# Kernel tuning notes

Hardware: AMD Instinct MI355X
Metric: run time of the kernel (lower is better)

The kernel has to match this reference:

```python
import jax, jax.numpy as jnp
import numpy as np

STRIDES = [(2, 2), (3, 3), (4, 4)]
EPS = 1e-5


def _conv1x1(x, w, b):
    # x: [B,C,H,W], w: [O,C] -> [B,O,H,W]
    return jnp.einsum('bchw,oc->bohw', x, w) + b[None, :, None, None]


def _stitch(x, hs, ws):
    # x: [B,dk,H,W] -> patches [B, hs*ws, dk*oh*ow]; patch index = i*ws + j matches
    # torch.stack over itertools.product(range(hs), range(ws)) of x[:,:,i::hs,j::ws]
    b, dk, H, W = x.shape
    oh, ow = H // hs, W // ws
    p = x.reshape(b, dk, oh, hs, ow, ws).transpose(0, 3, 5, 1, 2, 4)  # [B,hs,ws,dk,oh,ow]
    return p.reshape(b, hs * ws, dk * oh * ow)


def _unstitch(y, b, dk, hs, ws, oh, ow):
    # faithful to the torch permute(0,3,1,4,2,5): H is assembled as (hs, oh), W as (ws, ow)
    y = y.reshape(b, hs, ws, dk, oh, ow).transpose(0, 3, 1, 4, 2, 5)  # [B,dk,hs,oh,ws,ow]
    return y.reshape(b, dk, hs * oh, ws * ow)


def _attention(q, k, v):
    d = q.shape[-1]
    scores = jnp.einsum('bpd,bqd->bpq', q, k) / jnp.sqrt(jnp.asarray(d, q.dtype))
    p = jax.nn.softmax(scores, axis=-1)
    return jnp.einsum('bpq,bqd->bpd', p, v)


def _forward(x, wq, bq, wk, bk, wv, bv, w_out, b_out, gamma, beta):
    b, c, h, w = x.shape
    n = len(STRIDES)
    dk = c // n
    q = _conv1x1(x, wq, bq)
    k = _conv1x1(x, wk, bk)
    v = _conv1x1(x, wv, bv)
    outs = []
    for idx, (ws_, hs_) in enumerate(STRIDES):
        sl = slice(idx * dk, (idx + 1) * dk)
        oh, ow = h // hs_, w // ws_
        qp = _stitch(q[:, sl], hs_, ws_)
        kp = _stitch(k[:, sl], hs_, ws_)
        vp = _stitch(v[:, sl], hs_, ws_)
        y = _attention(qp, kp, vp)  # [B, hs*ws, dk*oh*ow]
        outs.append(_unstitch(y, b, dk, hs_, ws_, oh, ow))
    out = jnp.concatenate(outs, axis=1)  # [B,C,H,W]
    # output_linear: Conv3x3 -> BatchNorm2d (training-mode batch stats) -> LeakyReLU(0.2)
    y = jax.lax.conv_general_dilated(out, w_out, (1, 1), 'SAME',
                                     dimension_numbers=('NCHW', 'OIHW', 'NCHW'))
    y = y + b_out[None, :, None, None]
    mean = jnp.mean(y, axis=(0, 2, 3), keepdims=True)
    var = jnp.var(y, axis=(0, 2, 3), keepdims=True)
    y = (y - mean) * jax.lax.rsqrt(var + EPS)
    y = y * gamma[None, :, None, None] + beta[None, :, None, None]
    return jnp.where(y >= 0, y, 0.2 * y)


def setup_inputs() -> dict:
    key = jax.random.key(0)
    ks = jax.random.split(key, 10)
    B, C, H, W = 16, 192, 96, 96
    s = 0.02
    return {
        'x': jax.random.normal(ks[0], (B, C, H, W), jnp.float32),
        'wq': jax.random.normal(ks[1], (C, C), jnp.float32) * s,
        'bq': jnp.zeros((C,), jnp.float32),
        'wk': jax.random.normal(ks[2], (C, C), jnp.float32) * s,
        'bk': jnp.zeros((C,), jnp.float32),
        'wv': jax.random.normal(ks[3], (C, C), jnp.float32) * s,
        'bv': jnp.zeros((C,), jnp.float32),
        'w_out': jax.random.normal(ks[4], (C, C, 3, 3), jnp.float32) * s,
        'b_out': jnp.zeros((C,), jnp.float32),
        'gamma': jnp.ones((C,), jnp.float32),
        'beta': jnp.zeros((C,), jnp.float32),
    }


def reference(x, wq, bq, wk, bk, wv, bv, w_out, b_out, gamma, beta):
    return _forward(x, wq, bq, wk, bk, wv, bv, w_out, b_out, gamma, beta)
```

## Files before the change

### kernel.cpp

```cpp
#include <hip/hip_runtime.h>
#include <hip/hip_bf16.h>

#define BB 16
#define CC 192
#define HH 96
#define WWW 96
#define HWSZ 9216
#define DKC 64

typedef __hip_bfloat16 bf16;
typedef __attribute__((ext_vector_type(8))) short s8v;
typedef __attribute__((ext_vector_type(4))) float f32x4;

__device__ __forceinline__ float bf2f(unsigned short u) {
  union { unsigned int i; float f; } x; x.i = ((unsigned int)u) << 16; return x.f;
}
__device__ __forceinline__ unsigned short f2bf(float f) {
  union { __hip_bfloat16 h; unsigned short u; } c; c.h = __float2bfloat16(f); return c.u;
}

__global__ __launch_bounds__(256) void prep_w_kernel(const float* __restrict__ w_out,
                                                     unsigned short* __restrict__ wb9T) {
  int e = blockIdx.x * 256 + threadIdx.x;
  if (e >= 9 * CC * CC) return;
  int c = e % CC;
  int oc = (e / CC) % CC;
  int sh = e / (CC * CC);
  wb9T[e] = f2bf(w_out[((size_t)(oc * CC + c)) * 9 + sh]);
}

__global__ __launch_bounds__(256) void prep_wqkv_kernel(
    const float* __restrict__ wq, const float* __restrict__ wk, const float* __restrict__ wv,
    unsigned short* __restrict__ wqkv) {
  int e = blockIdx.x * 256 + threadIdx.x;
  if (e >= 3 * CC * CC) return;
  int sel = e / (CC * CC), r = e % (CC * CC);
  const float* w = sel == 0 ? wq : sel == 1 ? wk : wv;
  wqkv[e] = f2bf(w[r]);
}

__global__ __launch_bounds__(256) void xcvt_kernel(const float* __restrict__ x,
                                                   unsigned short* __restrict__ xb) {
  __shared__ float xt[CC][65];
  int b = blockIdx.x / 144, tile = blockIdx.x % 144;
  int pix0 = tile * 64;
  const float* xsrc = x + (size_t)b * CC * HWSZ + pix0;
  for (int e = threadIdx.x; e < CC * 16; e += 256) {
    int c = e >> 4, seg = e & 15;
    float4 t4 = *(const float4*)(xsrc + (size_t)c * HWSZ + seg * 4);
    xt[c][seg * 4 + 0] = t4.x; xt[c][seg * 4 + 1] = t4.y;
    xt[c][seg * 4 + 2] = t4.z; xt[c][seg * 4 + 3] = t4.w;
  }
  __syncthreads();
  unsigned short* dst = xb + ((size_t)(b * HWSZ + pix0)) * CC;
  for (int e = threadIdx.x; e < 24 * 64; e += 256) {
    int cg = e >> 6, p = e & 63;
    uint4 ov;
    unsigned short* ou = (unsigned short*)&ov;
    #pragma unroll
    for (int j = 0; j < 8; ++j) ou[j] = f2bf(xt[cg * 8 + j][p]);
    *(uint4*)(dst + (size_t)p * CC + cg * 8) = ov;
  }
}

#define VTS 232
__global__ __launch_bounds__(256) void qkv_mfma_kernel(
    const unsigned short* __restrict__ xb, const unsigned short* __restrict__ wqkv,
    const float* __restrict__ bq, const float* __restrict__ bk, const float* __restrict__ bv,
    unsigned short* __restrict__ q, unsigned short* __restrict__ k,
    unsigned short* __restrict__ v) {
  __shared__ unsigned short xl[96 * 200];
  __shared__ unsigned short vt[48 * VTS];
  const int tid = threadIdx.x;
  const int bid = (blockIdx.x & 7) * 192 + (blockIdx.x >> 3);
  const int h = bid % HH;
  const int b = bid / HH;
  const int lane = tid & 63, wid = tid >> 6;
  const int lr = lane & 15, hi8 = (lane >> 4) * 8, rowb = (lane >> 4) * 4;
  const int n0 = wid * 48;
  const unsigned short* xrow = xb + ((size_t)(b * HWSZ + h * WWW)) * CC;

  #pragma unroll
  for (int i = 0; i < 9; ++i) {
    int u = tid + i * 256;
    int pix = u / 24, cg = u % 24;
    *(uint4*)(xl + pix * 200 + cg * 8) = *(const uint4*)(xrow + (size_t)pix * CC + cg * 8);
  }
  __syncthreads();

  for (int sel = 0; sel < 3; ++sel) {
    const unsigned short* wsel = wqkv + (size_t)sel * CC * CC;
    f32x4 acc[6][3];
    #pragma unroll
    for (int mt = 0; mt < 6; ++mt)
      #pragma unroll
      for (int nt = 0; nt < 3; ++nt) acc[mt][nt] = (f32x4){0.f, 0.f, 0.f, 0.f};

    auto loadB = [&](int ck, s8v (&dst)[3]) {
      const unsigned short* src = wsel + ck * 32 + hi8;
      #pragma unroll
      for (int nt = 0; nt < 3; ++nt)
        dst[nt] = *(const s8v*)(src + (size_t)(n0 + nt * 16 + lr) * CC);
    };
    auto loadA = [&](int ck, s8v (&dst)[6]) {
      #pragma unroll
      for (int mt = 0; mt < 6; ++mt)
        dst[mt] = *(const s8v*)(xl + (mt * 16 + lr) * 200 + ck * 32 + hi8);
    };
    auto qstep = [&](int ck, s8v (&slot)[3], s8v (&acur)[6], s8v (&anxt)[6]) {
      if (ck < 5) loadA(ck + 1, anxt);
      #pragma unroll
      for (int mt = 0; mt < 6; ++mt)
        #pragma unroll
        for (int nt = 0; nt < 3; ++nt)
          acc[mt][nt] = __builtin_amdgcn_mfma_f32_16x16x32_bf16(acur[mt], slot[nt], acc[mt][nt], 0, 0, 0);
      if (ck + 3 < 6) loadB(ck + 3, slot);
    };

    s8v br0[3], br1[3], br2[3], aA[6], aB[6];
    loadB(0, br0); loadB(1, br1); loadB(2, br2);
    loadA(0, aA);
    qstep(0, br0, aA, aB);
    qstep(1, br1, aB, aA);
    qstep(2, br2, aA, aB);
    qstep(3, br0, aB, aA);
    qstep(4, br1, aA, aB);
    qstep(5, br2, aB, aA);

    const float* bsel = (sel == 0 ? bq : sel == 1 ? bk : bv);
    float bias[3];
    #pragma unroll
    for (int nt = 0; nt < 3; ++nt) bias[nt] = bsel[n0 + nt * 16 + lr];
    unsigned short* dst = (sel == 0 ? q : sel == 1 ? k : v) + ((size_t)(b * HWSZ + h * WWW)) * CC;
    #pragma unroll
    for (int pass = 0; pass < 2; ++pass) {
      __syncthreads();
      #pragma unroll
      for (int mt2 = 0; mt2 < 3; ++mt2)
        #pragma unroll
        for (int nt = 0; nt < 3; ++nt)
          #pragma unroll
          for (int i = 0; i < 4; ++i)
            vt[(mt2 * 16 + rowb + i) * VTS + n0 + nt * 16 + lr] =
                f2bf(acc[pass * 3 + mt2][nt][i] + bias[nt]);
      __syncthreads();
      for (int e = tid; e < 48 * 24; e += 256) {
        int p = e % 48, cg = e / 48;
        *(uint4*)(dst + (size_t)(pass * 48 + p) * CC + cg * 8) = *(uint4*)(vt + p * VTS + cg * 8);
      }
    }
  }
}

template <int HS, int WS, int OH, int OW, int IDX>
__global__ __launch_bounds__(256) void scores_mfma_kernel(
    const unsigned short* __restrict__ q, const unsigned short* __restrict__ k,
    float* __restrict__ scores) {
  constexpr int P = HS * WS;
  constexpr int NPOS = OH * OW;
  constexpr int SLABS = 64;
  constexpr int STRIDE = SLABS * 4;
  const int slab = blockIdx.x % SLABS;
  const int b = blockIdx.x / SLABS;
  const int wid = threadIdx.x >> 6;
  const int lane = threadIdx.x & 63;
  const int lr = lane & 15, g8 = (lane >> 4) * 8;
  const int p = (lr < P) ? lr : 0;
  const int pixoff = (p / WS) * WWW + (p % WS);
  const unsigned short* qb = q + (size_t)b * HWSZ * CC + IDX * 64 + g8;
  const unsigned short* kb = k + (size_t)b * HWSZ * CC + IDX * 64 + g8;

  f32x4 acc = (f32x4){0.f, 0.f, 0.f, 0.f};
  int rs = slab * 4 + wid;
  if (rs < NPOS) {
    s8v aq0, aq1, bk0, bk1;
    {
      int r = rs / OW, s = rs - r * OW;
      size_t pix = (size_t)(r * HS * WWW + s * WS + pixoff) * CC;
      aq0 = *(const s8v*)(qb + pix);
      aq1 = *(const s8v*)(qb + pix + 32);
      bk0 = *(const s8v*)(kb + pix);
      bk1 = *(const s8v*)(kb + pix + 32);
    }
    for (;;) {
      int nrs = rs + STRIDE;
      s8v nq0, nq1, nk0, nk1;
      if (nrs < NPOS) {
        int r = nrs / OW, s = nrs - r * OW;
        size_t pix = (size_t)(r * HS * WWW + s * WS + pixoff) * CC;
        nq0 = *(const s8v*)(qb + pix);
        nq1 = *(const s8v*)(qb + pix + 32);
        nk0 = *(const s8v*)(kb + pix);
        nk1 = *(const s8v*)(kb + pix + 32);
      }
      acc = __builtin_amdgcn_mfma_f32_16x16x32_bf16(aq0, bk0, acc, 0, 0, 0);
      acc = __builtin_amdgcn_mfma_f32_16x16x32_bf16(aq1, bk1, acc, 0, 0, 0);
      if (nrs >= NPOS) break;
      aq0 = nq0; aq1 = nq1; bk0 = nk0; bk1 = nk1;
      rs = nrs;
    }
  }
  const int col = lane & 15;
  const int row0 = (lane >> 4) * 4;
  if (col < P) {
    float* sc = scores + (IDX * BB + b) * 256;
    #pragma unroll
    for (int i = 0; i < 4; ++i) {
      int row = row0 + i;
      if (row < P) atomicAdd(sc + row * P + col, acc[i]);
    }
  }
}

__global__ void softmax_kernel(const float* __restrict__ scores, float* __restrict__ probs) {
  int t = threadIdx.x;
  int idx, b, p, P; float scale;
  if (t < 64)       { idx = 0; b = t >> 2;           p = t & 3;         P = 4;  scale = 1.f / 384.f; }
  else if (t < 208) { int u = t - 64;  idx = 1; b = u / 9;  p = u % 9;  P = 9;  scale = 1.f / 256.f; }
  else if (t < 464) { int u = t - 208; idx = 2; b = u >> 4; p = u & 15; P = 16; scale = 1.f / 192.f; }
  else return;
  const float* row = scores + (idx * BB + b) * 256 + p * P;
  float* orow = probs + (idx * BB + b) * 256 + p * P;
  float vals[16];
  float m = -1e30f;
  for (int i = 0; i < P; i++) { vals[i] = row[i] * scale; m = fmaxf(m, vals[i]); }
  float s = 0.f;
  for (int i = 0; i < P; i++) { vals[i] = expf(vals[i] - m); s += vals[i]; }
  float inv = 1.f / s;
  for (int i = 0; i < P; i++) orow[i] = vals[i] * inv;
}

template <int HS, int WS, int OH, int OW, int IDX>
__global__ __launch_bounds__(256) void pv_kernel(
    const unsigned short* __restrict__ v, const float* __restrict__ probs,
    unsigned short* __restrict__ attn) {
  constexpr int P = HS * WS;
  __shared__ unsigned short vl[HS * 96 * 72];
  __shared__ float pl[P * P];
  int b = blockIdx.x / OH;
  int r = blockIdx.x % OH;
  const int tid = threadIdx.x;
  for (int u = tid; u < HS * 96 * 8; u += 256) {
    int iq = u / 768, w = (u >> 3) % 96, cg = u & 7;
    *(uint4*)(vl + (iq * 96 + w) * 72 + cg * 8) =
        *(const uint4*)(v + ((size_t)(b * HWSZ + (r * HS + iq) * WWW + w)) * CC + IDX * 64 + cg * 8);
  }
  if (tid < P * P) pl[tid] = probs[(IDX * BB + b) * 256 + tid];
  __syncthreads();
  for (int u = tid; u < HS * 96 * 8; u += 256) {
    int i = u / 768, w = (u >> 3) % 96, cg = u & 7;
    int j = w / OW, s = w - j * OW;
    int p = i * WS + j;
    float acc[8];
    #pragma unroll
    for (int m = 0; m < 8; ++m) acc[m] = 0.f;
    #pragma unroll
    for (int iq = 0; iq < HS; ++iq) {
      #pragma unroll
      for (int jq = 0; jq < WS; ++jq) {
        float pw = pl[p * P + iq * WS + jq];
        s8v vv = *(const s8v*)(vl + (iq * 96 + s * WS + jq) * 72 + cg * 8);
        #pragma unroll
        for (int m = 0; m < 8; ++m) acc[m] += pw * bf2f((unsigned short)vv[m]);
      }
    }
    uint4 ov;
    ov.x = (unsigned int)f2bf(acc[0]) | ((unsigned int)f2bf(acc[1]) << 16);
    ov.y = (unsigned int)f2bf(acc[2]) | ((unsigned int)f2bf(acc[3]) << 16);
    ov.z = (unsigned int)f2bf(acc[4]) | ((unsigned int)f2bf(acc[5]) << 16);
    ov.w = (unsigned int)f2bf(acc[6]) | ((unsigned int)f2bf(acc[7]) << 16);
    *(uint4*)(attn + ((size_t)(b * HWSZ + (i * OH + r) * WWW + w)) * CC + IDX * 64 + cg * 8) = ov;
  }
}

__global__ __launch_bounds__(256) void conv_mfma_kernel(
    const unsigned short* __restrict__ attn, const unsigned short* __restrict__ wb9T,
    const float* __restrict__ b_out, unsigned short* __restrict__ ybf,
    float* __restrict__ bnsum, float* __restrict__ bnsqs) {
  __shared__ unsigned short al[3 * 98 * 40];
  const int tid = threadIdx.x;
  const int bid = (blockIdx.x & 7) * 192 + (blockIdx.x >> 3);
  const int h = bid % HH;
  const int b = bid / HH;
  const int lane = tid & 63, wid = tid >> 6;
  const int lr = lane & 15, hi8 = (lane >> 4) * 8, rowb = (lane >> 4) * 4;
  const int n0 = wid * 48;

  f32x4 acc[6][3];
  #pragma unroll
  for (int mt = 0; mt < 6; ++mt)
    #pragma unroll
    for (int nt = 0; nt < 3; ++nt) acc[mt][nt] = (f32x4){0.f, 0.f, 0.f, 0.f};

  uint4 aregs[5];
  auto stageA_LOAD = [&](int chunk) {
    int c0 = chunk * 32;
    #pragma unroll
    for (int i = 0; i < 5; ++i) {
      int u = tid + i * 256;
      if (u < 1176) {
        int row = u / 392, rem = u % 392, wx = rem >> 2, qq = rem & 3;
        int hr = h + row - 1, w = wx - 1;
        uint4 val = make_uint4(0u, 0u, 0u, 0u);
        if (hr >= 0 && hr < HH && w >= 0 && w < WWW)
          val = *(const uint4*)(attn + ((size_t)(b * HWSZ + hr * WWW + w)) * CC + c0 + qq * 8);
        aregs[i] = val;
      }
    }
  };
  auto stageA_WRITE = [&]() {
    #pragma unroll
    for (int i = 0; i < 5; ++i) {
      int u = tid + i * 256;
      if (u < 1176) {
        int row = u / 392, rem = u % 392, wx = rem >> 2, qq = rem & 3;
        *(uint4*)(al + (row * 98 + wx) * 40 + qq * 8) = aregs[i];
      }
    }
  };
  auto loadB = [&](int it2, s8v (&dst)[3]) {
    int chunk = it2 / 9, sh = it2 % 9;
    const unsigned short* src = wb9T + (size_t)sh * CC * CC + chunk * 32 + hi8;
    #pragma unroll
    for (int nt = 0; nt < 3; ++nt)
      dst[nt] = *(const s8v*)(src + (size_t)(n0 + nt * 16 + lr) * CC);
  };

  s8v br0[3], br1[3], br2[3];
  stageA_LOAD(0);
  stageA_WRITE();
  loadB(0, br0); loadB(1, br1); loadB(2, br2);
  __syncthreads();

  auto step = [&](int chunk, int sh, s8v (&slot)[3]) {
    if (sh == 0 && chunk < 5) stageA_LOAD(chunk + 1);
    int ky = sh / 3, kx = sh % 3;
    s8v a[6];
    #pragma unroll
    for (int mt = 0; mt < 6; ++mt)
      a[mt] = *(const s8v*)(al + (ky * 98 + mt * 16 + lr + kx) * 40 + hi8);
    #pragma unroll
    for (int mt = 0; mt < 6; ++mt)
      #pragma unroll
      for (int nt = 0; nt < 3; ++nt)
        acc[mt][nt] = __builtin_amdgcn_mfma_f32_16x16x32_bf16(a[mt], slot[nt], acc[mt][nt], 0, 0, 0);
    int it = chunk * 9 + sh;
    if (it + 3 < 54) loadB(it + 3, slot);
  };

  for (int chunk = 0; chunk < 6; ++chunk) {
    step(chunk, 0, br0);
    step(chunk, 1, br1);
    step(chunk, 2, br2);
    step(chunk, 3, br0);
    step(chunk, 4, br1);
    step(chunk, 5, br2);
    step(chunk, 6, br0);
    step(chunk, 7, br1);
    step(chunk, 8, br2);
    if (chunk < 5) {
      __syncthreads();
      stageA_WRITE();
      __syncthreads();
    }
  }

  #pragma unroll
  for (int nt = 0; nt < 3; ++nt) {
    int oc = n0 + nt * 16 + lr;
    float bias = b_out[oc];
    float s1 = 0.f, s2 = 0.f;
    #pragma unroll
    for (int mt = 0; mt < 6; ++mt) {
      float v0 = acc[mt][nt][0] + bias;
      float v1 = acc[mt][nt][1] + bias;
      float v2 = acc[mt][nt][2] + bias;
      float v3 = acc[mt][nt][3] + bias;
      s1 += v0 + v1 + v2 + v3;
      s2 += v0 * v0 + v1 * v1 + v2 * v2 + v3 * v3;
      uint2 pk;
      pk.x = (unsigned int)f2bf(v0) | ((unsigned int)f2bf(v1) << 16);
      pk.y = (unsigned int)f2bf(v2) | ((unsigned int)f2bf(v3) << 16);
      *(uint2*)(ybf + ((size_t)(b * CC + oc)) * HWSZ + h * WWW + mt * 16 + rowb) = pk;
    }
    s1 += __shfl_down(s1, 32);
    s1 += __shfl_down(s1, 16);
    s2 += __shfl_down(s2, 32);
    s2 += __shfl_down(s2, 16);
    if (lane < 16) {
      atomicAdd(bnsum + oc, s1);
      atomicAdd(bnsqs + oc, s2);
    }
  }
}

__global__ void bnfin_kernel(const float* __restrict__ bnsum, const float* __restrict__ bnsqs,
                             const float* __restrict__ gamma, const float* __restrict__ beta,
                             float* __restrict__ scale, float* __restrict__ shift) {
  int c = threadIdx.x;
  if (c >= CC) return;
  const float n = 16.f * 9216.f;
  float mean = bnsum[c] / n;
  float var = bnsqs[c] / n - mean * mean;
  float inv = rsqrtf(var + 1e-5f);
  float sc = gamma[c] * inv;
  scale[c] = sc;
  shift[c] = beta[c] - mean * sc;
}

__global__ __launch_bounds__(256) void bnapply_kernel(const unsigned short* __restrict__ ybf,
                                                      float* __restrict__ y,
                                                      const float* __restrict__ scale,
                                                      const float* __restrict__ shift) {
  const int total8 = BB * CC * HWSZ / 8;
  for (int e = blockIdx.x * 256 + threadIdx.x; e < total8; e += gridDim.x * 256) {
    uint4 t = ((const uint4*)ybf)[e];
    const unsigned short* u = (const unsigned short*)&t;
    int oc = (e / (HWSZ / 8)) % CC;
    float sc = scale[oc], sh = shift[oc];
    float4 o0, o1;
    float w;
    w = bf2f(u[0]) * sc + sh; o0.x = w >= 0.f ? w : 0.2f * w;
    w = bf2f(u[1]) * sc + sh; o0.y = w >= 0.f ? w : 0.2f * w;
    w = bf2f(u[2]) * sc + sh; o0.z = w >= 0.f ? w : 0.2f * w;
    w = bf2f(u[3]) * sc + sh; o0.w = w >= 0.f ? w : 0.2f * w;
    w = bf2f(u[4]) * sc + sh; o1.x = w >= 0.f ? w : 0.2f * w;
    w = bf2f(u[5]) * sc + sh; o1.y = w >= 0.f ? w : 0.2f * w;
    w = bf2f(u[6]) * sc + sh; o1.z = w >= 0.f ? w : 0.2f * w;
    w = bf2f(u[7]) * sc + sh; o1.w = w >= 0.f ? w : 0.2f * w;
    ((float4*)y)[e * 2] = o0;
    ((float4*)y)[e * 2 + 1] = o1;
  }
}

extern "C" void kernel_launch(void* const* d_in, const int* in_sizes, int n_in,
                              void* d_out, int out_size, void* d_ws, size_t ws_size,
                              hipStream_t stream) {
  const float* x     = (const float*)d_in[0];
  const float* wq    = (const float*)d_in[1];
  const float* bq    = (const float*)d_in[2];
  const float* wk    = (const float*)d_in[3];
  const float* bk    = (const float*)d_in[4];
  const float* wv    = (const float*)d_in[5];
  const float* bv    = (const float*)d_in[6];
  const float* w_out = (const float*)d_in[7];
  const float* b_out = (const float*)d_in[8];
  const float* gamma = (const float*)d_in[9];
  const float* beta  = (const float*)d_in[10];

  char* ws = (char*)d_ws;
  const size_t TB = (size_t)BB * CC * HWSZ * sizeof(bf16);
  unsigned short* q    = (unsigned short*)(ws);
  unsigned short* ybf  = q;
  unsigned short* k    = (unsigned short*)(ws + TB);
  unsigned short* v    = (unsigned short*)(ws + 2 * TB);
  unsigned short* attn = (unsigned short*)(ws + 3 * TB);
  unsigned short* xb   = attn;
  unsigned short* wb9T = (unsigned short*)(ws + 4 * TB);
  unsigned short* wqkv = (unsigned short*)(ws + 4 * TB + 663552);
  float* scores = (float*)(ws + 4 * TB + 663552 + 221184);
  float* bnsum  = scores + 3 * BB * 256;
  float* bnsqs  = bnsum + CC;
  float* probs  = bnsqs + CC;
  float* scale  = probs + 3 * BB * 256;
  float* shift  = scale + CC;
  float* y = (float*)d_out;

  hipMemsetAsync(scores, 0, 49152 + 2 * CC * 4, stream);

  prep_w_kernel<<<(9 * CC * CC + 255) / 256, 256, 0, stream>>>(w_out, wb9T);
  prep_wqkv_kernel<<<(3 * CC * CC + 255) / 256, 256, 0, stream>>>(wq, wk, wv, wqkv);

  xcvt_kernel<<<BB * 144, 256, 0, stream>>>(x, xb);
  qkv_mfma_kernel<<<BB * HH, 256, 0, stream>>>(xb, wqkv, bq, bk, bv, q, k, v);

  scores_mfma_kernel<2, 2, 48, 48, 0><<<BB * 64, 256, 0, stream>>>(q, k, scores);
  scores_mfma_kernel<3, 3, 32, 32, 1><<<BB * 64, 256, 0, stream>>>(q, k, scores);
  scores_mfma_kernel<4, 4, 24, 24, 2><<<BB * 64, 256, 0, stream>>>(q, k, scores);

  softmax_kernel<<<1, 512, 0, stream>>>(scores, probs);

  pv_kernel<2, 2, 48, 48, 0><<<BB * 48, 256, 0, stream>>>(v, probs, attn);
  pv_kernel<3, 3, 32, 32, 1><<<BB * 32, 256, 0, stream>>>(v, probs, attn);
  pv_kernel<4, 4, 24, 24, 2><<<BB * 24, 256, 0, stream>>>(v, probs, attn);

  conv_mfma_kernel<<<BB * HH, 256, 0, stream>>>(attn, wb9T, b_out, ybf, bnsum, bnsqs);

  bnfin_kernel<<<1, 256, 0, stream>>>(bnsum, bnsqs, gamma, beta, scale, shift);
  bnapply_kernel<<<2048, 256, 0, stream>>>(ybf, y, scale, shift);
}
```

Measured before the change: 436.7 us.

## Cut register pressure in qkv and conv kernels for three blocks per CU

Adds launch_bounds min-blocks 3 to the qkv and conv MFMA kernels. It shrinks the B-operand prefetch ring from three slots to two and drops the A double-buffer in qkv. It also replaces the LDS-transposed coalesced output store in qkv with direct scattered 2-byte global stores. The aim is higher occupancy from fewer VGPRs and less LDS, plus fewer barriers. The cost is a shallower prefetch distance and uncoalesced output writes.

```diff
diff --git a/kernel.cpp b/kernel.cpp
--- a/kernel.cpp
+++ b/kernel.cpp
@@ -63,14 +63,12 @@
   }
 }
 
-#define VTS 232
-__global__ __launch_bounds__(256) void qkv_mfma_kernel(
+__global__ __launch_bounds__(256, 3) void qkv_mfma_kernel(
     const unsigned short* __restrict__ xb, const unsigned short* __restrict__ wqkv,
     const float* __restrict__ bq, const float* __restrict__ bk, const float* __restrict__ bv,
     unsigned short* __restrict__ q, unsigned short* __restrict__ k,
     unsigned short* __restrict__ v) {
   __shared__ unsigned short xl[96 * 200];
-  __shared__ unsigned short vt[48 * VTS];
   const int tid = threadIdx.x;
   const int bid = (blockIdx.x & 7) * 192 + (blockIdx.x >> 3);
   const int h = bid % HH;
@@ -102,30 +100,24 @@
       for (int nt = 0; nt < 3; ++nt)
         dst[nt] = *(const s8v*)(src + (size_t)(n0 + nt * 16 + lr) * CC);
     };
-    auto loadA = [&](int ck, s8v (&dst)[6]) {
+    auto qstep = [&](int ck, s8v (&slot)[3]) {
+      s8v a[6];
       #pragma unroll
       for (int mt = 0; mt < 6; ++mt)
-        dst[mt] = *(const s8v*)(xl + (mt * 16 + lr) * 200 + ck * 32 + hi8);
-    };
-    auto qstep = [&](int ck, s8v (&slot)[3], s8v (&acur)[6], s8v (&anxt)[6]) {
-      if (ck < 5) loadA(ck + 1, anxt);
+        a[mt] = *(const s8v*)(xl + (mt * 16 + lr) * 200 + ck * 32 + hi8);
       #pragma unroll
       for (int mt = 0; mt < 6; ++mt)
         #pragma unroll
         for (int nt = 0; nt < 3; ++nt)
-          acc[mt][nt] = __builtin_amdgcn_mfma_f32_16x16x32_bf16(acur[mt], slot[nt], acc[mt][nt], 0, 0, 0);
-      if (ck + 3 < 6) loadB(ck + 3, slot);
+          acc[mt][nt] = __builtin_amdgcn_mfma_f32_16x16x32_bf16(a[mt], slot[nt], acc[mt][nt], 0, 0, 0);
+      if (ck + 2 < 6) loadB(ck + 2, slot);
     };
 
-    s8v br0[3], br1[3], br2[3], aA[6], aB[6];
-    loadB(0, br0); loadB(1, br1); loadB(2, br2);
-    loadA(0, aA);
-    qstep(0, br0, aA, aB);
-    qstep(1, br1, aB, aA);
-    qstep(2, br2, aA, aB);
-    qstep(3, br0, aB, aA);
-    qstep(4, br1, aA, aB);
-    qstep(5, br2, aB, aA);
+    s8v br0[3], br1[3];
+    loadB(0, br0); loadB(1, br1);
+    qstep(0, br0); qstep(1, br1);
+    qstep(2, br0); qstep(3, br1);
+    qstep(4, br0); qstep(5, br1);
 
     const float* bsel = (sel == 0 ? bq : sel == 1 ? bk : bv);
     float bias[3];
@@ -133,22 +125,13 @@
     for (int nt = 0; nt < 3; ++nt) bias[nt] = bsel[n0 + nt * 16 + lr];
     unsigned short* dst = (sel == 0 ? q : sel == 1 ? k : v) + ((size_t)(b * HWSZ + h * WWW)) * CC;
     #pragma unroll
-    for (int pass = 0; pass < 2; ++pass) {
-      __syncthreads();
-      #pragma unroll
-      for (int mt2 = 0; mt2 < 3; ++mt2)
+    for (int mt = 0; mt < 6; ++mt)
+      #pragma unroll
+      for (int nt = 0; nt < 3; ++nt)
         #pragma unroll
-        for (int nt = 0; nt < 3; ++nt)
-          #pragma unroll
-          for (int i = 0; i < 4; ++i)
-            vt[(mt2 * 16 + rowb + i) * VTS + n0 + nt * 16 + lr] =
-                f2bf(acc[pass * 3 + mt2][nt][i] + bias[nt]);
-      __syncthreads();
-      for (int e = tid; e < 48 * 24; e += 256) {
-        int p = e % 48, cg = e / 48;
-        *(uint4*)(dst + (size_t)(pass * 48 + p) * CC + cg * 8) = *(uint4*)(vt + p * VTS + cg * 8);
-      }
-    }
+        for (int i = 0; i < 4; ++i)
+          dst[(size_t)(mt * 16 + rowb + i) * CC + n0 + nt * 16 + lr] =
+              f2bf(acc[mt][nt][i] + bias[nt]);
   }
 }
 
@@ -273,7 +256,7 @@
   }
 }
 
-__global__ __launch_bounds__(256) void conv_mfma_kernel(
+__global__ __launch_bounds__(256, 3) void conv_mfma_kernel(
     const unsigned short* __restrict__ attn, const unsigned short* __restrict__ wb9T,
     const float* __restrict__ b_out, unsigned short* __restrict__ ybf,
     float* __restrict__ bnsum, float* __restrict__ bnsqs) {
@@ -326,13 +309,14 @@
       dst[nt] = *(const s8v*)(src + (size_t)(n0 + nt * 16 + lr) * CC);
   };
 
-  s8v br0[3], br1[3], br2[3];
+  s8v br0[3], br1[3];
   stageA_LOAD(0);
   stageA_WRITE();
-  loadB(0, br0); loadB(1, br1); loadB(2, br2);
+  loadB(0, br0); loadB(1, br1);
   __syncthreads();
 
-  auto step = [&](int chunk, int sh, s8v (&slot)[3]) {
+  auto step = [&](int it, s8v (&slot)[3]) {
+    int chunk = it / 9, sh = it % 9;
     if (sh == 0 && chunk < 5) stageA_LOAD(chunk + 1);
     int ky = sh / 3, kx = sh % 3;
     s8v a[6];
@@ -344,25 +328,16 @@
       #pragma unroll
       for (int nt = 0; nt < 3; ++nt)
         acc[mt][nt] = __builtin_amdgcn_mfma_f32_16x16x32_bf16(a[mt], slot[nt], acc[mt][nt], 0, 0, 0);
-    int it = chunk * 9 + sh;
-    if (it + 3 < 54) loadB(it + 3, slot);
-  };
-
-  for (int chunk = 0; chunk < 6; ++chunk) {
-    step(chunk, 0, br0);
-    step(chunk, 1, br1);
-    step(chunk, 2, br2);
-    step(chunk, 3, br0);
-    step(chunk, 4, br1);
-    step(chunk, 5, br2);
-    step(chunk, 6, br0);
-    step(chunk, 7, br1);
-    step(chunk, 8, br2);
-    if (chunk < 5) {
+    if (it + 2 < 54) loadB(it + 2, slot);
+    if (sh == 8 && chunk < 5) {
       __syncthreads();
       stageA_WRITE();
       __syncthreads();
     }
+  };
+  #pragma unroll
+  for (int it = 0; it < 54; ++it) {
+    if ((it & 1) == 0) step(it, br0); else step(it, br1);
   }
 
   #pragma unroll
```

After: 889.7 us. +103.7%, slower.
